# Optimization experiments

Measured on AMD Instinct MI355X. Metric: run time of the kernel, lower is better.

## Reference

```python
import jax, jax.numpy as jnp
import numpy as np

B, N, D, H = 512, 129, 256, 8   # batch, nodes (128 customers + depot), d_model, heads
HD = D // H                      # head_depth = 32
T = 128                          # decode steps
CLIP = 10.0                      # tanh_clipping
CAP = 1.0                        # VRPproblem.VEHICLE_CAPACITY


def setup_inputs() -> dict:
    key = jax.random.key(0)
    ks = jax.random.split(key, 9)
    s = 1.0 / np.sqrt(D)  # dense-layer init scale, keeps tanh logits unsaturated
    return {
        "embeddings": jax.random.normal(ks[0], (B, N, D), jnp.float32),
        "context_vectors": jax.random.normal(ks[1], (B, D), jnp.float32),
        "demands": jax.random.uniform(ks[2], (B, N), jnp.float32) * 0.1,
        "Wq_context": jax.random.normal(ks[3], (D, D), jnp.float32) * s,
        "Wq_step": jax.random.normal(ks[4], (D + 1, D), jnp.float32) * s,
        "Wk": jax.random.normal(ks[5], (D, D), jnp.float32) * s,
        "Wk_tanh": jax.random.normal(ks[6], (D, D), jnp.float32) * s,
        "Wv": jax.random.normal(ks[7], (D, D), jnp.float32) * s,
        "Wo": jax.random.normal(ks[8], (D, D), jnp.float32) * s,
    }


def _decode(embeddings, context_vectors, demands, Wq_context, Wq_step, Wk, Wk_tanh, Wv, Wo):
    b, n, dm = embeddings.shape
    hd = dm // H
    neg_inf = jnp.float32(-jnp.inf)
    # Precomputed once per rollout (as in the original call())
    K = (embeddings @ Wk).reshape(b, n, H, hd).transpose(0, 2, 1, 3)    # [b,H,n,hd]
    V = (embeddings @ Wv).reshape(b, n, H, hd).transpose(0, 2, 1, 3)    # [b,H,n,hd]
    Kt = embeddings @ Wk_tanh                                            # [b,n,dm]
    Qc = context_vectors @ Wq_context                                    # [b,dm]
    node_ids = jnp.arange(n)

    def step(carry, _):
        prev, used, visited = carry  # [b] int32, [b] f32, [b,n] bool (True = masked)
        # get_step_context: gather prev-node embedding, append remaining capacity
        cur = jnp.take_along_axis(embeddings, prev[:, None, None], axis=1)[:, 0]  # [b,dm]
        ctx = jnp.concatenate([cur, CAP - used[:, None]], axis=-1)                # [b,dm+1]
        Q = (Qc + ctx @ Wq_step).reshape(b, H, hd)                                # split heads, seq=1
        # decoder_mha: note original divides by head_depth (not sqrt)
        compat = jnp.einsum('bhd,bhnd->bhn', Q, K) / jnp.float32(hd)
        compat = jnp.where(visited[:, None, :], neg_inf, compat)
        attn = jnp.einsum('bhn,bhnd->bhd', jax.nn.softmax(compat, axis=-1), V)
        glimpse = attn.reshape(b, dm) @ Wo                                        # w_out
        # get_log_p: tanh-clipped pointer logits over all nodes
        logits = jnp.tanh(jnp.einsum('bd,bnd->bn', glimpse, Kt) / jnp.sqrt(jnp.float32(dm))) * CLIP
        logits = jnp.where(visited, neg_inf, logits)
        log_p = jax.nn.log_softmax(logits, axis=-1)                               # [b,n]
        # greedy _select_node + clip to valid range
        sel = jnp.clip(jnp.argmax(log_p, axis=-1).astype(jnp.int32), 0, n - 1)
        # state.step: visit node (depot index 0 always stays feasible), capacity update
        dem = jnp.take_along_axis(demands, sel[:, None], axis=1)[:, 0]
        used2 = jnp.where(sel == 0, jnp.float32(0.0), used + dem)
        visited2 = jnp.where(node_ids[None, :] == sel[:, None], sel[:, None] != 0, visited)
        return (sel, used2, visited2), (log_p, sel)

    init = (jnp.zeros((b,), jnp.int32), jnp.zeros((b,), jnp.float32), jnp.zeros((b, n), bool))
    _, (lp, pi) = jax.lax.scan(step, init, None, length=T)
    return lp.transpose(1, 0, 2), pi.T  # [b,T,n], [b,T]


def reference(embeddings, context_vectors, demands, Wq_context, Wq_step, Wk, Wk_tanh, Wv, Wo):
    log_probs, pi = _decode(embeddings, context_vectors, demands,
                            Wq_context, Wq_step, Wk, Wk_tanh, Wv, Wo)
    return log_probs, pi.astype(jnp.float32)
```

## Files before the change

### kernel.cpp

```cpp
#include <hip/hip_runtime.h>
#include <math.h>

#define NB 512
#define NN 129
#define DMM 256
#define NH 8
#define HDm 32
#define TT 128

#define PI_OFF ((size_t)NB * TT * NN)

#define NEG_SENTINEL (-1.0e30f)

#define EQ_SZ ((size_t)NB * NN * DMM)
#define V_OFF (EQ_SZ)
#define W2_OFF (2 * EQ_SZ)
#define QC_OFF (2 * EQ_SZ + (size_t)DMM * DMM)

__device__ __forceinline__ float tanh_fast(float x) {
  return 1.0f - 2.0f / (__expf(2.0f * x) + 1.0f);
}

__global__ __launch_bounds__(256) void w2_kernel(const float* __restrict__ Wkt,
                                                 const float* __restrict__ Wo,
                                                 float* __restrict__ W2) {
  __shared__ __align__(16) float rowL[DMM];
  int d = blockIdx.x, i = threadIdx.x;
  rowL[i] = Wkt[d * DMM + i];
  __syncthreads();
  const float4* wo4 = (const float4*)(Wo + (size_t)i * DMM);
  const float4* r4 = (const float4*)rowL;
  float acc = 0.f;
  #pragma unroll 8
  for (int jq = 0; jq < DMM / 4; ++jq) {
    float4 a = r4[jq], bq = wo4[jq];
    acc += a.x * bq.x + a.y * bq.y + a.z * bq.z + a.w * bq.w;
  }
  W2[d * DMM + i] = acc;
}

__global__ __launch_bounds__(256) void qc_kernel(const float* __restrict__ ctx,
                                                 const float* __restrict__ Wqc,
                                                 float* __restrict__ Qc) {
  __shared__ __align__(16) float cL[DMM];
  int b = blockIdx.x, j = threadIdx.x;
  cL[j] = ctx[b * DMM + j];
  __syncthreads();
  float acc = 0.f;
  for (int i = 0; i < DMM; ++i) acc += cL[i] * Wqc[i * DMM + j];
  Qc[b * DMM + j] = acc;
}

__global__ __launch_bounds__(256) void eqv_kernel(const float* __restrict__ emb,
                                                  const float* __restrict__ Wqs,
                                                  const float* __restrict__ Wv,
                                                  float* __restrict__ Eq,
                                                  float* __restrict__ Vws) {
  __shared__ __align__(16) float eL[64][DMM];
  int j = threadIdx.x;
  size_t r0 = (size_t)blockIdx.x * 64;
  for (int k = 0; k < 64; ++k) eL[k][j] = emb[(r0 + k) * DMM + j];
  __syncthreads();
  float accE[64], accV[64];
  #pragma unroll
  for (int r = 0; r < 64; ++r) { accE[r] = 0.f; accV[r] = 0.f; }
  for (int iq = 0; iq < 64; ++iq) {
    float we[4], wv[4];
    #pragma unroll
    for (int k = 0; k < 4; ++k) {
      we[k] = Wqs[(iq * 4 + k) * DMM + j];
      wv[k] = Wv[(iq * 4 + k) * DMM + j];
    }
    #pragma unroll
    for (int r = 0; r < 64; ++r) {
      float4 e = *(const float4*)&eL[r][iq * 4];
      accE[r] += e.x * we[0] + e.y * we[1] + e.z * we[2] + e.w * we[3];
      accV[r] += e.x * wv[0] + e.y * wv[1] + e.z * wv[2] + e.w * wv[3];
    }
  }
  for (int r = 0; r < 64; ++r) {
    Eq[(r0 + r) * DMM + j] = accE[r];
    Vws[(r0 + r) * DMM + j] = accV[r];
  }
}

__global__ __launch_bounds__(512, 2) void decode_kernel(
    const float* __restrict__ emb, const float* __restrict__ demands,
    const float* __restrict__ Wk, const float* __restrict__ Wqs,
    const float* __restrict__ Eq, const float* __restrict__ W2,
    const float* __restrict__ Qc, const float* __restrict__ Vws,
    float* __restrict__ out) {
  extern __shared__ float sm[];
  float* K128L = sm;
  float* T128L = sm + 256;
  float* V128L = sm + 512;
  float* demL = sm + 768;
  float* SCR = sm + 904;
  float* embL = SCR;
  float* WkT = SCR + 33156;
  float* W2T = SCR + 33156 + 2048;
  float* qL = SCR;
  float* pm = SCR + 256;
  float* attnL = SCR + 1312;
  float* ypd = SCR + 1568;

  const int tid = threadIdx.x;
  const int b = blockIdx.x;
  const int w = tid >> 6;
  const int l = tid & 63;
  const int dv = l & 31, h2 = l >> 5;

  const float* embB = emb + (size_t)b * NN * DMM;

  for (int idx = tid; idx < NN * DMM; idx += 512) {
    int r = idx >> 8, c = idx & 255;
    embL[r * 257 + c] = embB[idx];
  }
  if (tid < 132) demL[tid] = (tid < NN) ? demands[b * NN + tid] : 0.f;
  __syncthreads();

  if (tid < 256) {
    float a0 = 0.f, a1 = 0.f;
    for (int i = 0; i < DMM; ++i) {
      float e = embL[128 * 257 + i];
      a0 += e * Wk[i * DMM + tid];
      a1 += e * W2[i * DMM + tid];
    }
    K128L[tid] = a0;
    T128L[tid] = a1;
    V128L[tid] = Vws[((size_t)b * NN + 128) * DMM + tid];
  }

  float Kr0[HDm], Kr1[HDm], Tr0[HDm], Tr1[HDm];
  #pragma unroll
  for (int d = 0; d < HDm; ++d) { Kr0[d] = 0.f; Kr1[d] = 0.f; Tr0[d] = 0.f; Tr1[d] = 0.f; }
  for (int it = 0; it < 32; ++it) {
    __syncthreads();
    for (int idx = tid; idx < 2048; idx += 512) {
      WkT[idx] = Wk[it * 2048 + idx];
      W2T[idx] = W2[it * 2048 + idx];
    }
    __syncthreads();
    for (int i = 0; i < 8; ++i) {
      float e0 = embL[l * 257 + it * 8 + i];
      float e1 = embL[(l + 64) * 257 + it * 8 + i];
      const float4* wk4 = (const float4*)(WkT + i * DMM + w * HDm);
      const float4* w24 = (const float4*)(W2T + i * DMM + w * HDm);
      #pragma unroll
      for (int c = 0; c < 8; ++c) {
        float4 kv = wk4[c], tv = w24[c];
        Kr0[4*c+0] += e0 * kv.x; Kr0[4*c+1] += e0 * kv.y; Kr0[4*c+2] += e0 * kv.z; Kr0[4*c+3] += e0 * kv.w;
        Kr1[4*c+0] += e1 * kv.x; Kr1[4*c+1] += e1 * kv.y; Kr1[4*c+2] += e1 * kv.z; Kr1[4*c+3] += e1 * kv.w;
        Tr0[4*c+0] += e0 * tv.x; Tr0[4*c+1] += e0 * tv.y; Tr0[4*c+2] += e0 * tv.z; Tr0[4*c+3] += e0 * tv.w;
        Tr1[4*c+0] += e1 * tv.x; Tr1[4*c+1] += e1 * tv.y; Tr1[4*c+2] += e1 * tv.z; Tr1[4*c+3] += e1 * tv.w;
      }
    }
  }

  float Vr[64];
  {
    const float* vb = Vws + ((size_t)b * NN + h2 * 64) * DMM + w * HDm + dv;
    #pragma unroll
    for (int jj = 0; jj < 64; ++jj) Vr[jj] = vb[(size_t)jj * DMM];
  }

  float qcR = Qc[b * DMM + w * HDm + dv];
  float wqR = Wqs[256 * DMM + w * HDm + dv];
  float eqR = Eq[((size_t)b * NN + 0) * DMM + w * HDm + dv];

  float used = 0.f;
  int vis0 = 0, vis1 = 0, vis128 = 0;
  __syncthreads();

  float* outB = out + (size_t)b * TT * NN;

  for (int t = 0; t < TT; ++t) {
    float qd = qcR + eqR + (1.0f - used) * wqR;
    if (l < 32) qL[w * HDm + l] = qd;

    float s0, s1, s2;
    {
      const float4* q4 = (const float4*)(qL + w * HDm);
      const float4* k4 = (const float4*)(K128L + w * HDm);
      float a0 = 0.f, a1 = 0.f, a2 = 0.f, a3 = 0.f;
      float b0 = 0.f, b1 = 0.f, b2 = 0.f, b3 = 0.f;
      float c0 = 0.f, c1 = 0.f, c2 = 0.f, c3 = 0.f;
      #pragma unroll
      for (int c = 0; c < 8; ++c) {
        float4 q = q4[c], k = k4[c];
        a0 += q.x * Kr0[4*c];   a1 += q.y * Kr0[4*c+1];
        a2 += q.z * Kr0[4*c+2]; a3 += q.w * Kr0[4*c+3];
        b0 += q.x * Kr1[4*c];   b1 += q.y * Kr1[4*c+1];
        b2 += q.z * Kr1[4*c+2]; b3 += q.w * Kr1[4*c+3];
        c0 += q.x * k.x; c1 += q.y * k.y; c2 += q.z * k.z; c3 += q.w * k.w;
      }
      s0 = ((a0 + a1) + (a2 + a3)) * 0.03125f;
      s1 = ((b0 + b1) + (b2 + b3)) * 0.03125f;
      s2 = ((c0 + c1) + (c2 + c3)) * 0.03125f;
    }
    if (vis0) s0 = -INFINITY;
    if (vis1) s1 = -INFINITY;
    float e0 = __expf(s0), e1 = __expf(s1);
    float e2 = (l == 0 && !vis128) ? __expf(s2) : 0.f;
    float sum = e0 + e1 + e2;
    #pragma unroll
    for (int o = 32; o > 0; o >>= 1) sum += __shfl_xor(sum, o);
    float inv = 1.f / sum;
    pm[w * 132 + l] = e0 * inv;
    pm[w * 132 + 64 + l] = e1 * inv;
    if (l == 0) pm[w * 132 + 128] = e2 * inv;

    float acc;
    {
      const float4* pr = (const float4*)(pm + w * 132 + h2 * 64);
      float a0 = 0.f, a1 = 0.f, a2 = 0.f, a3 = 0.f;
      #pragma unroll
      for (int jq = 0; jq < 16; ++jq) {
        float4 p4 = pr[jq];
        a0 += p4.x * Vr[4*jq];   a1 += p4.y * Vr[4*jq+1];
        a2 += p4.z * Vr[4*jq+2]; a3 += p4.w * Vr[4*jq+3];
      }
      acc = (a0 + a1) + (a2 + a3);
    }
    if (h2 == 0) acc += pm[w * 132 + 128] * V128L[w * HDm + dv];
    acc += __shfl_xor(acc, 32);
    if (l < 32) attnL[w * HDm + l] = acc;

    float* ypb = ypd + (t & 1) * 1056;
    float y0, y1;
    {
      const float4* a4 = (const float4*)(attnL + w * HDm);
      float a0 = 0.f, a1 = 0.f, a2 = 0.f, a3 = 0.f;
      float b0 = 0.f, b1 = 0.f, b2 = 0.f, b3 = 0.f;
      #pragma unroll
      for (int c = 0; c < 8; ++c) {
        float4 a = a4[c];
        a0 += a.x * Tr0[4*c];   a1 += a.y * Tr0[4*c+1];
        a2 += a.z * Tr0[4*c+2]; a3 += a.w * Tr0[4*c+3];
        b0 += a.x * Tr1[4*c];   b1 += a.y * Tr1[4*c+1];
        b2 += a.z * Tr1[4*c+2]; b3 += a.w * Tr1[4*c+3];
      }
      y0 = (a0 + a1) + (a2 + a3);
      y1 = (b0 + b1) + (b2 + b3);
    }
    ypb[w * 132 + l] = y0;
    ypb[w * 132 + 64 + l] = y1;
    {
      float yy = 0.f;
      if (l < 8) {
        float4 a = ((const float4*)(attnL + w * HDm))[l];
        float4 tq = ((const float4*)(T128L + w * HDm))[l];
        yy = a.x * tq.x + a.y * tq.y + a.z * tq.z + a.w * tq.w;
      }
      yy += __shfl_xor(yy, 4);
      yy += __shfl_xor(yy, 2);
      yy += __shfl_xor(yy, 1);
      if (l == 0) ypb[w * 132 + 128] = yy;
    }

    __syncthreads();

    const float* yp = ypd + (t & 1) * 1056;
    float ya = 0.f, yb = 0.f, ys = 0.f;
    #pragma unroll
    for (int ww = 0; ww < 8; ++ww) {
      ya += yp[ww * 132 + l];
      yb += yp[ww * 132 + 64 + l];
      ys += yp[ww * 132 + 128];
    }
    float ra = vis0 ? -INFINITY : ya;
    float rb = vis1 ? -INFINITY : yb;
    float rc = (l == 0 && !vis128) ? ys : -INFINITY;

    float bv = ra;
    int bi = l;
    if (rb > bv) { bv = rb; bi = l + 64; }
    if (rc > bv) { bv = rc; bi = 128; }
    #pragma unroll
    for (int o = 32; o > 0; o >>= 1) {
      float ov = __shfl_xor(bv, o);
      int oi = __shfl_xor(bi, o);
      if (ov > bv || (ov == bv && oi < bi)) { bv = ov; bi = oi; }
    }
    const int sel = bi;
    float eqNew = Eq[((size_t)b * NN + sel) * DMM + w * HDm + dv];
    float dmv = demL[sel];

    if (w == 0) {
      float ta = vis0 ? -INFINITY : 10.f * tanh_fast(ya * 0.0625f);
      float tb = vis1 ? -INFINITY : 10.f * tanh_fast(yb * 0.0625f);
      float tc = (l == 0 && !vis128) ? 10.f * tanh_fast(ys * 0.0625f) : -INFINITY;
      float mv = 10.f * tanh_fast(bv * 0.0625f);
      float ea = __expf(ta - mv), eb = __expf(tb - mv);
      float ec = (l == 0) ? __expf(tc - mv) : 0.f;
      float se = ea + eb + ec;
      #pragma unroll
      for (int o = 32; o > 0; o >>= 1) se += __shfl_xor(se, o);
      float lse = mv + __logf(se);
      float* op = outB + (size_t)t * NN;
      op[l] = fmaxf(ta - lse, NEG_SENTINEL);
      op[l + 64] = fmaxf(tb - lse, NEG_SENTINEL);
      if (l == 0) {
        op[128] = fmaxf(tc - lse, NEG_SENTINEL);
        out[PI_OFF + (size_t)b * TT + t] = (float)sel;
      }
    }

    used = (sel == 0) ? 0.f : used + dmv;
    if (sel == l && sel != 0) vis0 = 1;
    if (sel == l + 64) vis1 = 1;
    if (sel == 128) vis128 = 1;
    eqR = eqNew;
  }
}

extern "C" void kernel_launch(void* const* d_in, const int* in_sizes, int n_in,
                              void* d_out, int out_size, void* d_ws, size_t ws_size,
                              hipStream_t stream) {
  const float* emb = (const float*)d_in[0];
  const float* ctx = (const float*)d_in[1];
  const float* dem = (const float*)d_in[2];
  const float* Wqc = (const float*)d_in[3];
  const float* Wqs = (const float*)d_in[4];
  const float* Wk = (const float*)d_in[5];
  const float* Wkt = (const float*)d_in[6];
  const float* Wv = (const float*)d_in[7];
  const float* Wo = (const float*)d_in[8];
  float* out = (float*)d_out;
  float* ws = (float*)d_ws;

  float* Eq = ws;
  float* Vws = ws + V_OFF;
  float* W2 = ws + W2_OFF;
  float* Qc = ws + QC_OFF;

  w2_kernel<<<dim3(DMM), dim3(DMM), 0, stream>>>(Wkt, Wo, W2);
  qc_kernel<<<dim3(NB), dim3(DMM), 0, stream>>>(ctx, Wqc, Qc);
  eqv_kernel<<<dim3((NB * NN) / 64), dim3(256), 0, stream>>>(emb, Wqs, Wv, Eq, Vws);

  const int SMEM = 38156 * 4;
  hipFuncSetAttribute(reinterpret_cast<const void*>(decode_kernel),
                      hipFuncAttributeMaxDynamicSharedMemorySize, SMEM);
  decode_kernel<<<dim3(NB), dim3(512), SMEM, stream>>>(emb, dem, Wk, Wqs, Eq, W2, Qc,
                                                       Vws, out);
}
```

Baseline: 1.375 ms.

## Stage Eq rows in LDS, defer softmax normalization, drop max in logsumexp

The per-block Eq slab is copied into shared memory once, reusing the embedding scratch region, so the per-step gather of the selected node's row comes from LDS instead of global memory. The attention softmax normalization is deferred: unnormalized exponentials are written, and the wavefront sum reduction is overlapped with the PV product before a single scale. The final log-softmax drops the max subtraction because tanh-clipped logits are bounded by 10, removing the dependency on the argmax value. The trade-offs are a larger upfront copy and the loss of max-shift protection, which relies on the clipping bound holding.

```diff
diff --git a/kernel.cpp b/kernel.cpp
--- a/kernel.cpp
+++ b/kernel.cpp
@@ -96,13 +96,15 @@
   float* V128L = sm + 512;
   float* demL = sm + 768;
   float* SCR = sm + 904;
+  float* SCR2 = SCR + 33156;
   float* embL = SCR;
-  float* WkT = SCR + 33156;
-  float* W2T = SCR + 33156 + 2048;
-  float* qL = SCR;
-  float* pm = SCR + 256;
-  float* attnL = SCR + 1312;
-  float* ypd = SCR + 1568;
+  float* WkT = SCR2;
+  float* W2T = SCR2 + 2048;
+  float* EqL = SCR;
+  float* qL = SCR2;
+  float* pm = SCR2 + 256;
+  float* attnL = SCR2 + 1312;
+  float* ypd = SCR2 + 1568;
 
   const int tid = threadIdx.x;
   const int b = blockIdx.x;
@@ -168,6 +170,15 @@
   float wqR = Wqs[256 * DMM + w * HDm + dv];
   float eqR = Eq[((size_t)b * NN + 0) * DMM + w * HDm + dv];
 
+  __syncthreads();
+  {
+    const float* EqB = Eq + (size_t)b * NN * DMM;
+    for (int idx = tid; idx < NN * DMM; idx += 512) {
+      int r = idx >> 8, c = idx & 255;
+      EqL[r * 257 + c] = EqB[idx];
+    }
+  }
+
   float used = 0.f;
   int vis0 = 0, vis1 = 0, vis128 = 0;
   __syncthreads();
@@ -202,13 +213,10 @@
     if (vis1) s1 = -INFINITY;
     float e0 = __expf(s0), e1 = __expf(s1);
     float e2 = (l == 0 && !vis128) ? __expf(s2) : 0.f;
-    float sum = e0 + e1 + e2;
-    #pragma unroll
-    for (int o = 32; o > 0; o >>= 1) sum += __shfl_xor(sum, o);
-    float inv = 1.f / sum;
-    pm[w * 132 + l] = e0 * inv;
-    pm[w * 132 + 64 + l] = e1 * inv;
-    if (l == 0) pm[w * 132 + 128] = e2 * inv;
+    pm[w * 132 + l] = e0;
+    pm[w * 132 + 64 + l] = e1;
+    if (l == 0) pm[w * 132 + 128] = e2;
+    float psum = e0 + e1 + e2;
 
     float acc;
     {
@@ -223,7 +231,10 @@
       acc = (a0 + a1) + (a2 + a3);
     }
     if (h2 == 0) acc += pm[w * 132 + 128] * V128L[w * HDm + dv];
+    #pragma unroll
+    for (int o = 32; o > 0; o >>= 1) psum += __shfl_xor(psum, o);
     acc += __shfl_xor(acc, 32);
+    acc *= (1.0f / psum);
     if (l < 32) attnL[w * HDm + l] = acc;
 
     float* ypb = ypd + (t & 1) * 1056;
@@ -283,20 +294,19 @@
       if (ov > bv || (ov == bv && oi < bi)) { bv = ov; bi = oi; }
     }
     const int sel = bi;
-    float eqNew = Eq[((size_t)b * NN + sel) * DMM + w * HDm + dv];
+    float eqNew = EqL[sel * 257 + w * HDm + dv];
     float dmv = demL[sel];
 
     if (w == 0) {
       float ta = vis0 ? -INFINITY : 10.f * tanh_fast(ya * 0.0625f);
       float tb = vis1 ? -INFINITY : 10.f * tanh_fast(yb * 0.0625f);
       float tc = (l == 0 && !vis128) ? 10.f * tanh_fast(ys * 0.0625f) : -INFINITY;
-      float mv = 10.f * tanh_fast(bv * 0.0625f);
-      float ea = __expf(ta - mv), eb = __expf(tb - mv);
-      float ec = (l == 0) ? __expf(tc - mv) : 0.f;
+      float ea = __expf(ta), eb = __expf(tb);
+      float ec = (l == 0 && !vis128) ? __expf(tc) : 0.f;
       float se = ea + eb + ec;
       #pragma unroll
       for (int o = 32; o > 0; o >>= 1) se += __shfl_xor(se, o);
-      float lse = mv + __logf(se);
+      float lse = __logf(se);
       float* op = outB + (size_t)t * NN;
       op[l] = fmaxf(ta - lse, NEG_SENTINEL);
       op[l + 64] = fmaxf(tb - lse, NEG_SENTINEL);
```

New measurement: 1.417 ms. 1.03x slower.
